# Kernel tuning notes

Hardware: AMD Instinct MI355X
Metric: run time of the kernel (lower is better)

## Reference

```python
import jax, jax.numpy as jnp
import numpy as np


def setup_inputs() -> dict:
    key = jax.random.key(0)
    k1, k2 = jax.random.split(key)
    B, C, H, W = 8, 128, 96, 160
    x1 = jax.random.normal(k1, (B, C, H, W), dtype=jnp.float32)
    x2 = jax.random.normal(k2, (B, C, H, W), dtype=jnp.float32)
    return {"x1": x1, "x2": x2, "d": 4}


def reference(x1, x2, d):
    # x1, x2: (B, C, H, W); output: (B, (2d+1)^2, H, W)
    b, c, h, w = x1.shape
    x2p = jnp.pad(x2, ((0, 0), (0, 0), (d, d), (d, d)))
    # Loop over the small fixed (2d+1)^2 displacement set (81 for d=4);
    # each term is a channel-reduced elementwise product (shift-multiply-sum).
    corrs = [
        jnp.einsum("bchw,bchw->bhw", x1,
                   jax.lax.dynamic_slice(x2p, (0, 0, i, j), (b, c, h, w)))
        for i in range(2 * d + 1)
        for j in range(2 * d + 1)
    ]
    out = jnp.stack(corrs, axis=1)  # (B, (2d+1)^2, H, W)
    return out / c
```

## Files before the change

### kernel.cpp

```cpp
#include <hip/hip_runtime.h>
#include <stdint.h>
#include <stddef.h>

#define Bb 8
#define Cc 128
#define Hh 96
#define Ww 160
#define HW (Hh*Ww)
#define Kk 81

typedef __attribute__((ext_vector_type(8))) short short8;
typedef __attribute__((ext_vector_type(4))) float floatx4;
typedef __attribute__((ext_vector_type(4))) unsigned int uintx4;

__device__ __forceinline__ uint32_t bf16rne(float f) {
  uint32_t u = __float_as_uint(f);
  return (u + 0x7FFFu + ((u >> 16) & 1u)) >> 16;
}

#define SBAR() __builtin_amdgcn_sched_barrier(0)


#define TPXF 1024
__global__ __launch_bounds__(256, 8)
void transpose_kernel(const float* __restrict__ x1, const float* __restrict__ x2,
                      ushort* __restrict__ x1t, ushort* __restrict__ x2t) {
  const int t   = threadIdx.x;
  const int b   = blockIdx.y;
  const int px0 = blockIdx.x * TPXF;
  const int zz  = blockIdx.z;
  const int cg  = zz & 15;
  const float* src = (zz >> 4) ? x2 : x1;
  ushort*      dst = (zz >> 4) ? x2t : x1t;

  const float* sb = src + (size_t)(b * Cc + cg * 8) * HW + px0 + t * 4;
  floatx4 v0 = *(const floatx4*)(sb + (size_t)0 * HW);
  floatx4 v1 = *(const floatx4*)(sb + (size_t)1 * HW);
  floatx4 v2 = *(const floatx4*)(sb + (size_t)2 * HW);
  floatx4 v3 = *(const floatx4*)(sb + (size_t)3 * HW);
  floatx4 v4 = *(const floatx4*)(sb + (size_t)4 * HW);
  floatx4 v5 = *(const floatx4*)(sb + (size_t)5 * HW);
  floatx4 v6 = *(const floatx4*)(sb + (size_t)6 * HW);
  floatx4 v7 = *(const floatx4*)(sb + (size_t)7 * HW);
  SBAR();

  ushort* dbase = dst + (((size_t)b * 16 + cg) * HW + px0 + t * 4) * 8;
#pragma unroll
  for (int j = 0; j < 4; ++j) {
    uintx4 q = (uintx4){bf16rne(v0[j]) | (bf16rne(v1[j]) << 16),
                        bf16rne(v2[j]) | (bf16rne(v3[j]) << 16),
                        bf16rne(v4[j]) | (bf16rne(v5[j]) << 16),
                        bf16rne(v6[j]) | (bf16rne(v7[j]) << 16)};
    *(uintx4*)&dbase[(size_t)j * 8] = q;
  }
}

__device__ __forceinline__ int clampi(int v, int lo, int hi) {
  return v < lo ? lo : (v > hi ? hi : v);
}

#define CKSTEP ((long)4 * HW * 8)

#define LOADRAW(dst, tt, ckc)                                                  \
  dst = *(const short8*)&base2c[rowoff##tt + (ckc) * CKSTEP];

#define ZSEL(v, tt)                                                            \
  v = (okw && (unsigned)(gh2b + (tt)) < (unsigned)Hh) ? v                      \
      : (short8){0, 0, 0, 0, 0, 0, 0, 0};

__global__ __launch_bounds__(256, 3)
void corr_t3_kernel(const ushort* __restrict__ x1t, const ushort* __restrict__ x2t,
                    float* __restrict__ out) {
  __shared__ float ldsOut[Kk * 66];

  const int tid  = threadIdx.x;
  const int flat = blockIdx.x;
  const int b  = flat & 7;
  const int j  = flat >> 3;
  const int by = j / 10;
  const int bx = j - by * 10;
  const int w0 = bx * 16;
  const int h0 = by * 4;

  const int lane = tid & 63;
  const int wv   = tid >> 6;
  const int vy = wv & 1, vx = wv >> 1;
  const int n = lane & 15, quad = lane >> 4;
  const int s = n >> 3, pw = n & 7;

  floatx4 acc[10];
#pragma unroll
  for (int t = 0; t < 10; ++t) acc[t] = (floatx4){0.f, 0.f, 0.f, 0.f};

  const int gw2  = w0 - 4 + 8 * vx + n;
  const bool okw = (unsigned)gw2 < (unsigned)Ww;
  const int gw2c = clampi(gw2, 0, Ww - 1);
  const int gh2b = h0 - 4 + 2 * vy;

  const ushort* base2c = x2t + (((long)b * 16 + quad) * HW + gw2c) * 8;
  const ushort* base1  = x1t + (((long)b * 16 + quad) * HW
                                + (long)(h0 + 2 * vy + s) * Ww
                                + (w0 + 8 * vx + pw)) * 8;

  const long rowoff0 = (long)clampi(gh2b + 0, 0, Hh - 1) * (Ww * 8);
  const long rowoff1 = (long)clampi(gh2b + 1, 0, Hh - 1) * (Ww * 8);
  const long rowoff2 = (long)clampi(gh2b + 2, 0, Hh - 1) * (Ww * 8);
  const long rowoff3 = (long)clampi(gh2b + 3, 0, Hh - 1) * (Ww * 8);
  const long rowoff4 = (long)clampi(gh2b + 4, 0, Hh - 1) * (Ww * 8);
  const long rowoff5 = (long)clampi(gh2b + 5, 0, Hh - 1) * (Ww * 8);
  const long rowoff6 = (long)clampi(gh2b + 6, 0, Hh - 1) * (Ww * 8);
  const long rowoff7 = (long)clampi(gh2b + 7, 0, Hh - 1) * (Ww * 8);
  const long rowoff8 = (long)clampi(gh2b + 8, 0, Hh - 1) * (Ww * 8);
  const long rowoff9 = (long)clampi(gh2b + 9, 0, Hh - 1) * (Ww * 8);

  const short8 bf0 = *(const short8*)&base1[0 * CKSTEP];
  const short8 bf1 = *(const short8*)&base1[1 * CKSTEP];
  const short8 bf2 = *(const short8*)&base1[2 * CKSTEP];
  const short8 bf3 = *(const short8*)&base1[3 * CKSTEP];

  short8 aA0, aA1, aA2, aA3, aA4, aA5, aA6, aA7, aA8, aA9;
  short8 aB0, aB1, aB2, aB3, aB4, aB5, aB6, aB7, aB8, aB9;

  LOADRAW(aA0, 0, 0); LOADRAW(aA1, 1, 0); LOADRAW(aA2, 2, 0); LOADRAW(aA3, 3, 0);
  LOADRAW(aA4, 4, 0); LOADRAW(aA5, 5, 0); LOADRAW(aA6, 6, 0); LOADRAW(aA7, 7, 0);
  LOADRAW(aA8, 8, 0); LOADRAW(aA9, 9, 0);
  SBAR();
  LOADRAW(aB0, 0, 1); LOADRAW(aB1, 1, 1); LOADRAW(aB2, 2, 1); LOADRAW(aB3, 3, 1);
  LOADRAW(aB4, 4, 1); LOADRAW(aB5, 5, 1); LOADRAW(aB6, 6, 1); LOADRAW(aB7, 7, 1);
  LOADRAW(aB8, 8, 1); LOADRAW(aB9, 9, 1);
  SBAR();
  ZSEL(aA0, 0); ZSEL(aA1, 1); ZSEL(aA2, 2); ZSEL(aA3, 3); ZSEL(aA4, 4);
  ZSEL(aA5, 5); ZSEL(aA6, 6); ZSEL(aA7, 7); ZSEL(aA8, 8); ZSEL(aA9, 9);
  acc[0] = __builtin_amdgcn_mfma_f32_16x16x32_bf16(aA0, bf0, acc[0], 0, 0, 0);
  acc[1] = __builtin_amdgcn_mfma_f32_16x16x32_bf16(aA1, bf0, acc[1], 0, 0, 0);
  acc[2] = __builtin_amdgcn_mfma_f32_16x16x32_bf16(aA2, bf0, acc[2], 0, 0, 0);
  acc[3] = __builtin_amdgcn_mfma_f32_16x16x32_bf16(aA3, bf0, acc[3], 0, 0, 0);
  acc[4] = __builtin_amdgcn_mfma_f32_16x16x32_bf16(aA4, bf0, acc[4], 0, 0, 0);
  acc[5] = __builtin_amdgcn_mfma_f32_16x16x32_bf16(aA5, bf0, acc[5], 0, 0, 0);
  acc[6] = __builtin_amdgcn_mfma_f32_16x16x32_bf16(aA6, bf0, acc[6], 0, 0, 0);
  acc[7] = __builtin_amdgcn_mfma_f32_16x16x32_bf16(aA7, bf0, acc[7], 0, 0, 0);
  acc[8] = __builtin_amdgcn_mfma_f32_16x16x32_bf16(aA8, bf0, acc[8], 0, 0, 0);
  acc[9] = __builtin_amdgcn_mfma_f32_16x16x32_bf16(aA9, bf0, acc[9], 0, 0, 0);
  SBAR();
  LOADRAW(aA0, 0, 2); LOADRAW(aA1, 1, 2); LOADRAW(aA2, 2, 2); LOADRAW(aA3, 3, 2);
  LOADRAW(aA4, 4, 2); LOADRAW(aA5, 5, 2); LOADRAW(aA6, 6, 2); LOADRAW(aA7, 7, 2);
  LOADRAW(aA8, 8, 2); LOADRAW(aA9, 9, 2);
  SBAR();
  ZSEL(aB0, 0); ZSEL(aB1, 1); ZSEL(aB2, 2); ZSEL(aB3, 3); ZSEL(aB4, 4);
  ZSEL(aB5, 5); ZSEL(aB6, 6); ZSEL(aB7, 7); ZSEL(aB8, 8); ZSEL(aB9, 9);
  acc[0] = __builtin_amdgcn_mfma_f32_16x16x32_bf16(aB0, bf1, acc[0], 0, 0, 0);
  acc[1] = __builtin_amdgcn_mfma_f32_16x16x32_bf16(aB1, bf1, acc[1], 0, 0, 0);
  acc[2] = __builtin_amdgcn_mfma_f32_16x16x32_bf16(aB2, bf1, acc[2], 0, 0, 0);
  acc[3] = __builtin_amdgcn_mfma_f32_16x16x32_bf16(aB3, bf1, acc[3], 0, 0, 0);
  acc[4] = __builtin_amdgcn_mfma_f32_16x16x32_bf16(aB4, bf1, acc[4], 0, 0, 0);
  acc[5] = __builtin_amdgcn_mfma_f32_16x16x32_bf16(aB5, bf1, acc[5], 0, 0, 0);
  acc[6] = __builtin_amdgcn_mfma_f32_16x16x32_bf16(aB6, bf1, acc[6], 0, 0, 0);
  acc[7] = __builtin_amdgcn_mfma_f32_16x16x32_bf16(aB7, bf1, acc[7], 0, 0, 0);
  acc[8] = __builtin_amdgcn_mfma_f32_16x16x32_bf16(aB8, bf1, acc[8], 0, 0, 0);
  acc[9] = __builtin_amdgcn_mfma_f32_16x16x32_bf16(aB9, bf1, acc[9], 0, 0, 0);
  SBAR();
  LOADRAW(aB0, 0, 3); LOADRAW(aB1, 1, 3); LOADRAW(aB2, 2, 3); LOADRAW(aB3, 3, 3);
  LOADRAW(aB4, 4, 3); LOADRAW(aB5, 5, 3); LOADRAW(aB6, 6, 3); LOADRAW(aB7, 7, 3);
  LOADRAW(aB8, 8, 3); LOADRAW(aB9, 9, 3);
  SBAR();
  ZSEL(aA0, 0); ZSEL(aA1, 1); ZSEL(aA2, 2); ZSEL(aA3, 3); ZSEL(aA4, 4);
  ZSEL(aA5, 5); ZSEL(aA6, 6); ZSEL(aA7, 7); ZSEL(aA8, 8); ZSEL(aA9, 9);
  acc[0] = __builtin_amdgcn_mfma_f32_16x16x32_bf16(aA0, bf2, acc[0], 0, 0, 0);
  acc[1] = __builtin_amdgcn_mfma_f32_16x16x32_bf16(aA1, bf2, acc[1], 0, 0, 0);
  acc[2] = __builtin_amdgcn_mfma_f32_16x16x32_bf16(aA2, bf2, acc[2], 0, 0, 0);
  acc[3] = __builtin_amdgcn_mfma_f32_16x16x32_bf16(aA3, bf2, acc[3], 0, 0, 0);
  acc[4] = __builtin_amdgcn_mfma_f32_16x16x32_bf16(aA4, bf2, acc[4], 0, 0, 0);
  acc[5] = __builtin_amdgcn_mfma_f32_16x16x32_bf16(aA5, bf2, acc[5], 0, 0, 0);
  acc[6] = __builtin_amdgcn_mfma_f32_16x16x32_bf16(aA6, bf2, acc[6], 0, 0, 0);
  acc[7] = __builtin_amdgcn_mfma_f32_16x16x32_bf16(aA7, bf2, acc[7], 0, 0, 0);
  acc[8] = __builtin_amdgcn_mfma_f32_16x16x32_bf16(aA8, bf2, acc[8], 0, 0, 0);
  acc[9] = __builtin_amdgcn_mfma_f32_16x16x32_bf16(aA9, bf2, acc[9], 0, 0, 0);
  SBAR();
  ZSEL(aB0, 0); ZSEL(aB1, 1); ZSEL(aB2, 2); ZSEL(aB3, 3); ZSEL(aB4, 4);
  ZSEL(aB5, 5); ZSEL(aB6, 6); ZSEL(aB7, 7); ZSEL(aB8, 8); ZSEL(aB9, 9);
  acc[0] = __builtin_amdgcn_mfma_f32_16x16x32_bf16(aB0, bf3, acc[0], 0, 0, 0);
  acc[1] = __builtin_amdgcn_mfma_f32_16x16x32_bf16(aB1, bf3, acc[1], 0, 0, 0);
  acc[2] = __builtin_amdgcn_mfma_f32_16x16x32_bf16(aB2, bf3, acc[2], 0, 0, 0);
  acc[3] = __builtin_amdgcn_mfma_f32_16x16x32_bf16(aB3, bf3, acc[3], 0, 0, 0);
  acc[4] = __builtin_amdgcn_mfma_f32_16x16x32_bf16(aB4, bf3, acc[4], 0, 0, 0);
  acc[5] = __builtin_amdgcn_mfma_f32_16x16x32_bf16(aB5, bf3, acc[5], 0, 0, 0);
  acc[6] = __builtin_amdgcn_mfma_f32_16x16x32_bf16(aB6, bf3, acc[6], 0, 0, 0);
  acc[7] = __builtin_amdgcn_mfma_f32_16x16x32_bf16(aB7, bf3, acc[7], 0, 0, 0);
  acc[8] = __builtin_amdgcn_mfma_f32_16x16x32_bf16(aB8, bf3, acc[8], 0, 0, 0);
  acc[9] = __builtin_amdgcn_mfma_f32_16x16x32_bf16(aB9, bf3, acc[9], 0, 0, 0);

  const float scale = 1.0f / 128.0f;
  const int prow = 2 * vy + s;
  const int pcol = 8 * vx + pw;
#pragma unroll
  for (int t = 0; t < 10; ++t) {
    int di = t - 4 - s;
    if ((unsigned)(di + 4) > 8u) continue;
#pragma unroll
    for (int r = 0; r < 4; ++r) {
      int dj = quad * 4 + r - 4 - pw;
      if ((unsigned)(dj + 4) > 8u) continue;
      int kk = (di + 4) * 9 + (dj + 4);
      ldsOut[kk * 66 + prow * 16 + pcol] = acc[t][r] * scale;
    }
  }
  __syncthreads();

  for (int idx = tid; idx < Kk * 64; idx += 256) {
    int kk  = idx >> 6;
    int rem = idx & 63;
    int hh  = rem >> 4;
    int ww  = rem & 15;
    out[((size_t)b * Kk + kk) * HW + (size_t)(h0 + hh) * Ww + (w0 + ww)] =
        ldsOut[kk * 66 + rem];
  }
}

__global__ __launch_bounds__(512, 4)
void corr_kernel(const float* __restrict__ x1, const float* __restrict__ x2,
                 float* __restrict__ out) {
  __shared__ __align__(16) ushort ldsX2[16*24*40];
  __shared__ __align__(16) ushort ldsX1[8*16*40];

  const int tid = threadIdx.x;
  const int flat = blockIdx.x;
  const int b  = flat & 7;
  const int j  = flat >> 3;
  const int by = j / 10;
  const int bx = j - by * 10;
  const int w0 = bx * 16;
  const int h0 = by * 8;

  const int lane = tid & 63;
  const int wv   = tid >> 6;
  const int vy = wv & 3, vx = wv >> 2;
  const int n = lane & 15, quad = lane >> 4;
  const int s = n >> 3, pw = n & 7;

  floatx4 acc[10];
#pragma unroll
  for (int t = 0; t < 10; ++t) acc[t] = (floatx4){0.f, 0.f, 0.f, 0.f};

  for (int ck = 0; ck < 4; ++ck) {
    const int c0 = ck * 32;
    if (ck) __syncthreads();

#pragma unroll
    for (int it = 0; it < 3; ++it) {
      int T   = it * 512 + tid;
      int w24 = T % 24;
      int t2  = T / 24;
      int rw  = t2 & 15;
      int cg  = t2 >> 4;
      int gh = h0 - 4 + rw;
      int gw = w0 - 4 + w24;
      bool ok = ((unsigned)gh < Hh) && ((unsigned)gw < Ww);
      const float* src = x2 + ((size_t)(b*Cc + c0 + cg*8) * HW + gh*Ww + gw);
      uint32_t p0, p1, p2, p3;
      {
        float a0 = ok ? src[0*HW] : 0.f;
        float a1 = ok ? src[1*HW] : 0.f;
        float a2 = ok ? src[2*HW] : 0.f;
        float a3 = ok ? src[3*HW] : 0.f;
        float a4 = ok ? src[4*HW] : 0.f;
        float a5 = ok ? src[5*HW] : 0.f;
        float a6 = ok ? src[6*HW] : 0.f;
        float a7 = ok ? src[7*HW] : 0.f;
        p0 = bf16rne(a0) | (bf16rne(a1) << 16);
        p1 = bf16rne(a2) | (bf16rne(a3) << 16);
        p2 = bf16rne(a4) | (bf16rne(a5) << 16);
        p3 = bf16rne(a6) | (bf16rne(a7) << 16);
      }
      *(uintx4*)&ldsX2[(rw*24 + w24)*40 + cg*8] = (uintx4){p0, p1, p2, p3};
    }

    {
      int T  = tid;
      int wl = T & 15;
      int t2 = T >> 4;
      int rl = t2 & 7;
      int cg = t2 >> 3;
      const float* src = x1 + ((size_t)(b*Cc + c0 + cg*8) * HW
                               + (h0 + rl)*Ww + (w0 + wl));
      uint32_t p0, p1, p2, p3;
      float a0 = src[0*HW], a1 = src[1*HW], a2 = src[2*HW], a3 = src[3*HW];
      float a4 = src[4*HW], a5 = src[5*HW], a6 = src[6*HW], a7 = src[7*HW];
      p0 = bf16rne(a0) | (bf16rne(a1) << 16);
      p1 = bf16rne(a2) | (bf16rne(a3) << 16);
      p2 = bf16rne(a4) | (bf16rne(a5) << 16);
      p3 = bf16rne(a6) | (bf16rne(a7) << 16);
      *(uintx4*)&ldsX1[(rl*16 + wl)*40 + cg*8] = (uintx4){p0, p1, p2, p3};
    }

    __syncthreads();

    short8 bfrag = *(const short8*)&ldsX1[((2*vy + s)*16 + 8*vx + pw)*40 + quad*8];
#pragma unroll
    for (int t = 0; t < 10; ++t) {
      short8 afrag = *(const short8*)&ldsX2[((2*vy + t)*24 + 8*vx + n)*40 + quad*8];
      acc[t] = __builtin_amdgcn_mfma_f32_16x16x32_bf16(afrag, bfrag, acc[t], 0, 0, 0);
    }
  }

  const float scale = 1.0f / 128.0f;
  const int ph  = h0 + 2*vy + s;
  const int pwg = w0 + 8*vx + pw;
#pragma unroll
  for (int t = 0; t < 10; ++t) {
    int di = t - 4 - s;
    if ((unsigned)(di + 4) > 8u) continue;
#pragma unroll
    for (int r = 0; r < 4; ++r) {
      int dj = quad*4 + r - 4 - pw;
      if ((unsigned)(dj + 4) > 8u) continue;
      int kk = (di + 4) * 9 + (dj + 4);
      out[((size_t)b*Kk + kk) * HW + ph*Ww + pwg] = acc[t][r] * scale;
    }
  }
}

extern "C" void kernel_launch(void* const* d_in, const int* in_sizes, int n_in,
                              void* d_out, int out_size, void* d_ws, size_t ws_size,
                              hipStream_t stream) {
  const float* x1 = (const float*)d_in[0];
  const float* x2 = (const float*)d_in[1];
  float* out = (float*)d_out;

  const size_t elems = (size_t)Bb * HW * Cc;
  const size_t need  = 2 * elems * sizeof(ushort);

  if (d_ws != nullptr && ws_size >= need) {
    ushort* x1t = (ushort*)d_ws;
    ushort* x2t = x1t + elems;
    transpose_kernel<<<dim3(HW / TPXF, Bb, 32), dim3(256, 1, 1), 0, stream>>>(
        x1, x2, x1t, x2t);
    corr_t3_kernel<<<dim3(1920, 1, 1), dim3(256, 1, 1), 0, stream>>>(x1t, x2t, out);
  } else {
    corr_kernel<<<dim3(960, 1, 1), dim3(512, 1, 1), 0, stream>>>(x1, x2, out);
  }
}
```

Measured before the change: 185.1 us.

## Fuse x1 bf16 conversion into correlation kernel via LDS staging

Removes x1 from the transpose pre-pass. The correlation kernel now loads x1 fp32 tiles directly, converts them to bf16 and stores them channel-last in shared memory for MFMA B fragments. This eliminates writing and re-reading a bf16 copy of x1 in global memory and halves the transpose work. It adds LDS usage, a block barrier and scalar 16-bit LDS stores that may conflict.

```diff
diff --git a/kernel.cpp b/kernel.cpp
--- a/kernel.cpp
+++ b/kernel.cpp
@@ -23,17 +23,13 @@
 
 #define TPXF 1024
 __global__ __launch_bounds__(256, 8)
-void transpose_kernel(const float* __restrict__ x1, const float* __restrict__ x2,
-                      ushort* __restrict__ x1t, ushort* __restrict__ x2t) {
+void transpose_kernel(const float* __restrict__ x2, ushort* __restrict__ x2t) {
   const int t   = threadIdx.x;
   const int b   = blockIdx.y;
   const int px0 = blockIdx.x * TPXF;
-  const int zz  = blockIdx.z;
-  const int cg  = zz & 15;
-  const float* src = (zz >> 4) ? x2 : x1;
-  ushort*      dst = (zz >> 4) ? x2t : x1t;
-
-  const float* sb = src + (size_t)(b * Cc + cg * 8) * HW + px0 + t * 4;
+  const int cg  = blockIdx.z;
+
+  const float* sb = x2 + (size_t)(b * Cc + cg * 8) * HW + px0 + t * 4;
   floatx4 v0 = *(const floatx4*)(sb + (size_t)0 * HW);
   floatx4 v1 = *(const floatx4*)(sb + (size_t)1 * HW);
   floatx4 v2 = *(const floatx4*)(sb + (size_t)2 * HW);
@@ -44,7 +40,7 @@
   floatx4 v7 = *(const floatx4*)(sb + (size_t)7 * HW);
   SBAR();
 
-  ushort* dbase = dst + (((size_t)b * 16 + cg) * HW + px0 + t * 4) * 8;
+  ushort* dbase = x2t + (((size_t)b * 16 + cg) * HW + px0 + t * 4) * 8;
 #pragma unroll
   for (int j = 0; j < 4; ++j) {
     uintx4 q = (uintx4){bf16rne(v0[j]) | (bf16rne(v1[j]) << 16),
@@ -60,6 +56,7 @@
 }
 
 #define CKSTEP ((long)4 * HW * 8)
+#define X1STR 136
 
 #define LOADRAW(dst, tt, ckc)                                                  \
   dst = *(const short8*)&base2c[rowoff##tt + (ckc) * CKSTEP];
@@ -69,9 +66,10 @@
       : (short8){0, 0, 0, 0, 0, 0, 0, 0};
 
 __global__ __launch_bounds__(256, 3)
-void corr_t3_kernel(const ushort* __restrict__ x1t, const ushort* __restrict__ x2t,
+void corr_t4_kernel(const float* __restrict__ x1, const ushort* __restrict__ x2t,
                     float* __restrict__ out) {
-  __shared__ float ldsOut[Kk * 66];
+  __shared__ float  ldsOut[Kk * 66];
+  __shared__ ushort ldsX1[64 * X1STR];
 
   const int tid  = threadIdx.x;
   const int flat = blockIdx.x;
@@ -88,6 +86,23 @@
   const int n = lane & 15, quad = lane >> 4;
   const int s = n >> 3, pw = n & 7;
 
+  {
+    const float* x1base = x1 + (size_t)(b * Cc) * HW + (size_t)h0 * Ww + w0;
+#pragma unroll
+    for (int it = 0; it < 8; ++it) {
+      int T   = it * 256 + tid;
+      int c   = T >> 4;
+      int rem = T & 15;
+      int r   = rem >> 2;
+      int q4  = rem & 3;
+      floatx4 v = *(const floatx4*)&x1base[(size_t)c * HW + r * Ww + q4 * 4];
+      int px = r * 16 + q4 * 4;
+#pragma unroll
+      for (int jj = 0; jj < 4; ++jj)
+        ldsX1[(px + jj) * X1STR + c] = (ushort)bf16rne(v[jj]);
+    }
+  }
+
   floatx4 acc[10];
 #pragma unroll
   for (int t = 0; t < 10; ++t) acc[t] = (floatx4){0.f, 0.f, 0.f, 0.f};
@@ -98,9 +113,6 @@
   const int gh2b = h0 - 4 + 2 * vy;
 
   const ushort* base2c = x2t + (((long)b * 16 + quad) * HW + gw2c) * 8;
-  const ushort* base1  = x1t + (((long)b * 16 + quad) * HW
-                                + (long)(h0 + 2 * vy + s) * Ww
-                                + (w0 + 8 * vx + pw)) * 8;
 
   const long rowoff0 = (long)clampi(gh2b + 0, 0, Hh - 1) * (Ww * 8);
   const long rowoff1 = (long)clampi(gh2b + 1, 0, Hh - 1) * (Ww * 8);
@@ -113,11 +125,6 @@
   const long rowoff8 = (long)clampi(gh2b + 8, 0, Hh - 1) * (Ww * 8);
   const long rowoff9 = (long)clampi(gh2b + 9, 0, Hh - 1) * (Ww * 8);
 
-  const short8 bf0 = *(const short8*)&base1[0 * CKSTEP];
-  const short8 bf1 = *(const short8*)&base1[1 * CKSTEP];
-  const short8 bf2 = *(const short8*)&base1[2 * CKSTEP];
-  const short8 bf3 = *(const short8*)&base1[3 * CKSTEP];
-
   short8 aA0, aA1, aA2, aA3, aA4, aA5, aA6, aA7, aA8, aA9;
   short8 aB0, aB1, aB2, aB3, aB4, aB5, aB6, aB7, aB8, aB9;
 
@@ -129,6 +136,15 @@
   LOADRAW(aB4, 4, 1); LOADRAW(aB5, 5, 1); LOADRAW(aB6, 6, 1); LOADRAW(aB7, 7, 1);
   LOADRAW(aB8, 8, 1); LOADRAW(aB9, 9, 1);
   SBAR();
+
+  __syncthreads();
+  const int pxl = (2 * vy + s) * 16 + 8 * vx + pw;
+  const short8 bf0 = *(const short8*)&ldsX1[pxl * X1STR +  0 + quad * 8];
+  const short8 bf1 = *(const short8*)&ldsX1[pxl * X1STR + 32 + quad * 8];
+  const short8 bf2 = *(const short8*)&ldsX1[pxl * X1STR + 64 + quad * 8];
+  const short8 bf3 = *(const short8*)&ldsX1[pxl * X1STR + 96 + quad * 8];
+  SBAR();
+
   ZSEL(aA0, 0); ZSEL(aA1, 1); ZSEL(aA2, 2); ZSEL(aA3, 3); ZSEL(aA4, 4);
   ZSEL(aA5, 5); ZSEL(aA6, 6); ZSEL(aA7, 7); ZSEL(aA8, 8); ZSEL(aA9, 9);
   acc[0] = __builtin_amdgcn_mfma_f32_16x16x32_bf16(aA0, bf0, acc[0], 0, 0, 0);
@@ -220,7 +236,7 @@
 void corr_kernel(const float* __restrict__ x1, const float* __restrict__ x2,
                  float* __restrict__ out) {
   __shared__ __align__(16) ushort ldsX2[16*24*40];
-  __shared__ __align__(16) ushort ldsX1[8*16*40];
+  __shared__ __align__(16) ushort ldsX1f[8*16*40];
 
   const int tid = threadIdx.x;
   const int flat = blockIdx.x;
@@ -289,12 +305,12 @@
       p1 = bf16rne(a2) | (bf16rne(a3) << 16);
       p2 = bf16rne(a4) | (bf16rne(a5) << 16);
       p3 = bf16rne(a6) | (bf16rne(a7) << 16);
-      *(uintx4*)&ldsX1[(rl*16 + wl)*40 + cg*8] = (uintx4){p0, p1, p2, p3};
+      *(uintx4*)&ldsX1f[(rl*16 + wl)*40 + cg*8] = (uintx4){p0, p1, p2, p3};
     }
 
     __syncthreads();
 
-    short8 bfrag = *(const short8*)&ldsX1[((2*vy + s)*16 + 8*vx + pw)*40 + quad*8];
+    short8 bfrag = *(const short8*)&ldsX1f[((2*vy + s)*16 + 8*vx + pw)*40 + quad*8];
 #pragma unroll
     for (int t = 0; t < 10; ++t) {
       short8 afrag = *(const short8*)&ldsX2[((2*vy + t)*24 + 8*vx + n)*40 + quad*8];
@@ -327,14 +343,13 @@
   float* out = (float*)d_out;
 
   const size_t elems = (size_t)Bb * HW * Cc;
-  const size_t need  = 2 * elems * sizeof(ushort);
+  const size_t need  = elems * sizeof(ushort);
 
   if (d_ws != nullptr && ws_size >= need) {
-    ushort* x1t = (ushort*)d_ws;
-    ushort* x2t = x1t + elems;
-    transpose_kernel<<<dim3(HW / TPXF, Bb, 32), dim3(256, 1, 1), 0, stream>>>(
-        x1, x2, x1t, x2t);
-    corr_t3_kernel<<<dim3(1920, 1, 1), dim3(256, 1, 1), 0, stream>>>(x1t, x2t, out);
+    ushort* x2t = (ushort*)d_ws;
+    transpose_kernel<<<dim3(HW / TPXF, Bb, 16), dim3(256, 1, 1), 0, stream>>>(
+        x2, x2t);
+    corr_t4_kernel<<<dim3(1920, 1, 1), dim3(256, 1, 1), 0, stream>>>(x1, x2t, out);
   } else {
     corr_kernel<<<dim3(960, 1, 1), dim3(512, 1, 1), 0, stream>>>(x1, x2, out);
   }
```

After: 185.6 us. No clear change (+0.3%).
